# Optimization experiments

Hardware: AMD Instinct MI355X
Metric: run time of the kernel (lower is better)

Reference implementation:

```python
import jax, jax.numpy as jnp
import numpy as np

B, S, F, D, H, DFF, C = 64, 1024, 136, 64, 2, 256, 2
DH = D // H


def sinusoidal_pe(seq_len, d_model):
    position = jnp.arange(seq_len, dtype=jnp.float32)[:, None]
    div_term = jnp.exp(jnp.arange(0, d_model, 2, dtype=jnp.float32) * (-np.log(10000.0) / d_model))
    ang = position * div_term  # [S, D/2]
    pe = jnp.zeros((seq_len, d_model), dtype=jnp.float32)
    pe = pe.at[:, 0::2].set(jnp.sin(ang))
    pe = pe.at[:, 1::2].set(jnp.cos(ang))
    return pe


def layer_norm(x, g, b, eps=1e-5):
    mu = jnp.mean(x, axis=-1, keepdims=True)
    var = jnp.mean(jnp.square(x - mu), axis=-1, keepdims=True)
    return (x - mu) * jax.lax.rsqrt(var + eps) * g + b


def setup_inputs() -> dict:
    key = jax.random.key(0)
    ks = jax.random.split(key, 16)
    r = lambda k, shape, scale: jax.random.normal(k, shape, dtype=jnp.float32) * scale
    return {
        'x': r(ks[0], (B, S, F), 1.0),
        'W_in': r(ks[1], (F, D), F ** -0.5), 'b_in': jnp.zeros((D,), jnp.float32),
        'W_qkv': r(ks[2], (D, 3 * D), D ** -0.5), 'b_qkv': jnp.zeros((3 * D,), jnp.float32),
        'W_o': r(ks[3], (D, D), D ** -0.5), 'b_o': jnp.zeros((D,), jnp.float32),
        'g1': jnp.ones((D,), jnp.float32), 'beta1': jnp.zeros((D,), jnp.float32),
        'W1': r(ks[4], (D, DFF), D ** -0.5), 'b1': jnp.zeros((DFF,), jnp.float32),
        'W2': r(ks[5], (DFF, D), DFF ** -0.5), 'b2': jnp.zeros((D,), jnp.float32),
        'g2': jnp.ones((D,), jnp.float32), 'beta2': jnp.zeros((D,), jnp.float32),
        'W_c1': r(ks[6], (D, D), D ** -0.5), 'b_c1': jnp.zeros((D,), jnp.float32),
        'W_c2': r(ks[7], (D, C), D ** -0.5), 'b_c2': jnp.zeros((C,), jnp.float32),
    }


def reference(x, W_in, b_in, W_qkv, b_qkv, W_o, b_o, g1, beta1, W1, b1, W2, b2, g2, beta2, W_c1, b_c1, W_c2, b_c2):
    # input projection + positional encoding
    h = x @ W_in + b_in                      # [B,S,D]
    h = h + sinusoidal_pe(h.shape[1], D)
    # multi-head self-attention with explicit weights (need_weights=True path)
    qkv = h @ W_qkv + b_qkv                  # [B,S,3D]
    q, k, v = jnp.split(qkv, 3, axis=-1)
    q = q.reshape(B, S, H, DH)
    k = k.reshape(B, S, H, DH)
    v = v.reshape(B, S, H, DH)
    scores = jnp.einsum('bihd,bjhd->bhij', q, k) / np.sqrt(DH)
    attn = jax.nn.softmax(scores, axis=-1)   # [B,H,S,S] per-head attention weights
    ctx = jnp.einsum('bhij,bjhd->bihd', attn, v).reshape(B, S, D)
    attn_out = ctx @ W_o + b_o
    # post-norm encoder layer (dropout inactive in eval)
    h = layer_norm(h + attn_out, g1, beta1)
    ff = jax.nn.relu(h @ W1 + b1) @ W2 + b2
    h = layer_norm(h + ff, g2, beta2)
    # mean pool + classifier
    pooled = jnp.mean(h, axis=1)             # [B,D]
    logits = jax.nn.relu(pooled @ W_c1 + b_c1) @ W_c2 + b_c2
    return logits, attn
```

## Files before the change

### kernel.cpp

```cpp
#include <hip/hip_runtime.h>


typedef unsigned short u16;
typedef short bf16x8 __attribute__((ext_vector_type(8)));
typedef short bf16x4 __attribute__((ext_vector_type(4)));
typedef float f32x4 __attribute__((ext_vector_type(4)));

#define DEVI __device__ __forceinline__
#define MFMA __builtin_amdgcn_mfma_f32_16x16x32_bf16

DEVI u16 f2bf(float f) {
  union { float f; unsigned u; } v; v.f = f;
  unsigned r = v.u + 0x7FFFu + ((v.u >> 16) & 1u);
  return (u16)(r >> 16);
}
DEVI float bf2f(u16 h) {
  union { unsigned u; float f; } v; v.u = ((unsigned)h) << 16;
  return v.f;
}
DEVI float wred_sum(float v) {
#pragma unroll
  for (int off = 32; off; off >>= 1) v += __shfl_xor(v, off);
  return v;
}

__global__ __launch_bounds__(256) void r1_inproj(const float* __restrict__ x,
                                                 const float* __restrict__ Win,
                                                 const float* __restrict__ bin,
                                                 float* __restrict__ hf) {
  __shared__ float xs[32][140];
  const int r0 = blockIdx.x * 32, t = threadIdx.x;
  const int lane = t & 63, wv = t >> 6;
  for (int e = t; e < 32 * 136; e += 256) {
    int r = e / 136, k = e - r * 136;
    xs[r][k] = x[(size_t)(r0 + r) * 136 + k];
  }
  __syncthreads();
  float acc[8];
#pragma unroll
  for (int r = 0; r < 8; ++r) acc[r] = 0.f;
  for (int k = 0; k < 136; k += 4) {
    float w0 = Win[(size_t)k * 64 + lane];
    float w1 = Win[(size_t)(k + 1) * 64 + lane];
    float w2 = Win[(size_t)(k + 2) * 64 + lane];
    float w3 = Win[(size_t)(k + 3) * 64 + lane];
#pragma unroll
    for (int r = 0; r < 8; ++r) {
      f32x4 xv = *(const f32x4*)&xs[wv * 8 + r][k];
      acc[r] = fmaf(xv[0], w0, fmaf(xv[1], w1, fmaf(xv[2], w2, fmaf(xv[3], w3, acc[r]))));
    }
  }
  const float bcol = bin[lane];
  const int m = lane >> 1;
  const float freq = __expf((float)(2 * m) * -0.14391156831212787f);
  const int s0 = r0 & 1023;
#pragma unroll
  for (int r = 0; r < 8; ++r) {
    const int row = wv * 8 + r;
    const float ang = (float)(s0 + row) * freq;
    const float pe = (lane & 1) ? cosf(ang) : sinf(ang);
    hf[(size_t)(r0 + row) * 64 + lane] = acc[r] + bcol + pe;
  }
}

__global__ __launch_bounds__(384) void r2_qkv(const float* __restrict__ hf,
                                              const float* __restrict__ Wq,
                                              const float* __restrict__ bq,
                                              u16* __restrict__ qH, u16* __restrict__ qL,
                                              u16* __restrict__ kH, u16* __restrict__ kL,
                                              u16* __restrict__ vtH, u16* __restrict__ vtL) {
  __shared__ float hr[32][68];
  __shared__ u16 vbH[64][40];
  __shared__ u16 vbL[64][40];
  const int r0 = blockIdx.x * 32, t = threadIdx.x;
  const int g = t / 192, u = t - g * 192;
  for (int e = t; e < 2048; e += 384) {
    int r = e >> 6, k = e & 63;
    hr[r][k] = hf[(size_t)(r0 + r) * 64 + k];
  }
  __syncthreads();
  float acc[16];
  const float bias = bq[u];
#pragma unroll
  for (int r = 0; r < 16; ++r) acc[r] = bias;
  for (int k = 0; k < 64; k += 4) {
    float w0 = Wq[(size_t)k * 192 + u];
    float w1 = Wq[(size_t)(k + 1) * 192 + u];
    float w2 = Wq[(size_t)(k + 2) * 192 + u];
    float w3 = Wq[(size_t)(k + 3) * 192 + u];
#pragma unroll
    for (int r = 0; r < 16; ++r) {
      f32x4 hv = *(const f32x4*)&hr[g * 16 + r][k];
      acc[r] = fmaf(hv[0], w0, fmaf(hv[1], w1, fmaf(hv[2], w2, fmaf(hv[3], w3, acc[r]))));
    }
  }
  const int which = u >> 6, c = u & 63, h = c >> 5, dh = c & 31;
  const int b = r0 >> 10, s0 = r0 & 1023;
  const size_t bh = (size_t)(b * 2 + h);
#pragma unroll
  for (int r = 0; r < 16; ++r) {
    const int row = g * 16 + r;
    const int s = s0 + row;
    u16 hi = f2bf(acc[r]);
    u16 lo = f2bf(acc[r] - bf2f(hi));
    if (which == 0)      { qH[(bh * 1024 + s) * 32 + dh] = hi; qL[(bh * 1024 + s) * 32 + dh] = lo; }
    else if (which == 1) { kH[(bh * 1024 + s) * 32 + dh] = hi; kL[(bh * 1024 + s) * 32 + dh] = lo; }
    else                 { vbH[c][row] = hi; vbL[c][row] = lo; }
  }
  __syncthreads();
  if (t < 128) {
    const int hh = (t & 63) >> 5, dh2 = t & 31;
    const size_t vb = ((size_t)(b * 2 + hh) * 32 + dh2) * 1024 + s0;
    const u16* src = (t < 64) ? &vbH[(t & 63)][0] : &vbL[(t & 63)][0];
    u16* dst = (t < 64) ? vtH : vtL;
#pragma unroll
    for (int i = 0; i < 2; ++i) {
      bf16x8 v = *(const bf16x8*)&src[i * 16];
      bf16x8 w = *(const bf16x8*)&src[i * 16 + 8];
      *(bf16x8*)&dst[vb + i * 16] = v;
      *(bf16x8*)&dst[vb + i * 16 + 8] = w;
    }
  }
}

__global__ __launch_bounds__(512, 4) void r3_fa(const u16* __restrict__ qH, const u16* __restrict__ qL,
                                                const u16* __restrict__ kH, const u16* __restrict__ kL,
                                                const u16* __restrict__ vtH, const u16* __restrict__ vtL,
                                                float* __restrict__ attn, float* __restrict__ ctx) {
  __shared__ __align__(16) char smem[33280];
  u16* pb = (u16*)smem;
  float* reds = (float*)(smem + 32768);
  float* part = (float*)smem;

  const int bid = blockIdx.x;
  const int wid = (bid & 7) * 1024 + (bid >> 3);
  const int bh = wid >> 6, qt = wid & 63;
  const int t = threadIdx.x, lane = t & 63, wv = t >> 6;
  const int fr = lane & 15, rg = lane >> 4, koff = rg * 8;
  const int i0 = qt * 16;
  const float scale = 0.17677669529663687f;

  const size_t qoff = ((size_t)bh * 1024 + i0 + fr) * 32 + koff;
  bf16x8 aqh = *(const bf16x8*)&qH[qoff];
  bf16x8 aql = *(const bf16x8*)&qL[qoff];

  f32x4 s[8];
#pragma unroll
  for (int jl = 0; jl < 8; ++jl) {
    const int jt = wv * 8 + jl;
    const size_t kof = ((size_t)bh * 1024 + jt * 16 + fr) * 32 + koff;
    bf16x8 bkh = *(const bf16x8*)&kH[kof];
    bf16x8 bkl = *(const bf16x8*)&kL[kof];
    f32x4 a = {};
    a = MFMA(aqh, bkh, a, 0, 0, 0);
    a = MFMA(aqh, bkl, a, 0, 0, 0);
    a = MFMA(aql, bkh, a, 0, 0, 0);
#pragma unroll
    for (int r = 0; r < 4; ++r) s[jl][r] = a[r] * scale;
  }

  float s4[4] = {0.f, 0.f, 0.f, 0.f};
#pragma unroll
  for (int jl = 0; jl < 8; ++jl)
#pragma unroll
    for (int r = 0; r < 4; ++r) { s[jl][r] = __expf(s[jl][r]); s4[r] += s[jl][r]; }
#pragma unroll
  for (int off = 1; off < 16; off <<= 1)
#pragma unroll
    for (int r = 0; r < 4; ++r) s4[r] += __shfl_xor(s4[r], off);
  if (fr == 0) {
#pragma unroll
    for (int r = 0; r < 4; ++r) reds[wv * 16 + rg * 4 + r] = s4[r];
  }
  __syncthreads();
  float inv[4];
#pragma unroll
  for (int r = 0; r < 4; ++r) {
    const int row = rg * 4 + r;
    float ssum = reds[row];
#pragma unroll
    for (int w = 1; w < 8; ++w) ssum += reds[w * 16 + row];
    inv[r] = 1.f / ssum;
  }

#pragma unroll
  for (int r = 0; r < 4; ++r) {
    const int row = rg * 4 + r;
    const int sw = rg << 4;
    const int rb = row * 1024;
#pragma unroll
    for (int jl = 0; jl < 8; jl += 2) {
      const float f0 = s[jl][r] * inv[r];
      const float f1 = s[jl + 1][r] * inv[r];
      unsigned pk;
      asm("v_cvt_pk_bf16_f32 %0, %1, %2" : "=v"(pk) : "v"(f0), "v"(f1));
      const int c0 = (wv * 8 + jl) * 16 + fr;
      pb[rb + (c0 ^ sw)] = (u16)pk;
      pb[rb + ((c0 + 16) ^ sw)] = (u16)(pk >> 16);
    }
  }
  __syncthreads();

  {
    const int row = t >> 5, x32 = t & 31;
    const int sw = (row >> 2) << 4;
    const size_t gb = ((size_t)bh * 1024 + i0 + row) * 1024;
#pragma unroll
    for (int c = 0; c < 8; ++c) {
      const int col = x32 * 4 + 128 * c;
      bf16x4 v = *(const bf16x4*)&pb[row * 1024 + (col ^ sw)];
      f32x4 o;
#pragma unroll
      for (int i = 0; i < 4; ++i) o[i] = bf2f((u16)v[i]);
      __builtin_nontemporal_store(o, (f32x4*)&attn[gb + col]);
    }
  }

  const int sw2 = (fr >> 2) << 4;
  f32x4 acc2[2] = {};
#pragma unroll
  for (int i = 0; i < 4; ++i) {
    const int kt = wv * 4 + i;
    const int cb = kt * 32 + rg * 8;
    bf16x8 ph = *(const bf16x8*)&pb[fr * 1024 + (cb ^ sw2)];
#pragma unroll
    for (int nb = 0; nb < 2; ++nb) {
      const size_t vo = ((size_t)bh * 32 + nb * 16 + fr) * 1024 + cb;
      bf16x8 vh = *(const bf16x8*)&vtH[vo];
      bf16x8 vl = *(const bf16x8*)&vtL[vo];
      acc2[nb] = MFMA(ph, vh, acc2[nb], 0, 0, 0);
      acc2[nb] = MFMA(ph, vl, acc2[nb], 0, 0, 0);
    }
  }
  __syncthreads();
#pragma unroll
  for (int nb = 0; nb < 2; ++nb)
#pragma unroll
    for (int r = 0; r < 4; ++r)
      part[(wv * 16 + rg * 4 + r) * 32 + nb * 16 + fr] = acc2[nb][r];
  __syncthreads();
  const int b = bh >> 1, h = bh & 1;
  {
    const int row = t >> 5, dh = t & 31;
    float v = part[(row) * 32 + dh];
#pragma unroll
    for (int w = 1; w < 8; ++w) v += part[(w * 16 + row) * 32 + dh];
    ctx[((size_t)b * 1024 + i0 + row) * 64 + h * 32 + dh] = v;
  }
}

__global__ __launch_bounds__(256) void r56_ln_ff(const float* __restrict__ ctx,
                                                 const float* __restrict__ Wo,
                                                 const float* __restrict__ bo,
                                                 const float* __restrict__ hf,
                                                 const float* __restrict__ g1,
                                                 const float* __restrict__ be1,
                                                 const float* __restrict__ W1,
                                                 const float* __restrict__ b1,
                                                 const float* __restrict__ W2,
                                                 const float* __restrict__ b2,
                                                 const float* __restrict__ g2,
                                                 const float* __restrict__ be2,
                                                 float* __restrict__ pp) {
  __shared__ __align__(16) char smem[38656];
  float* yr   = (float*)smem;
  float* fr   = (float*)(smem + 4352);
  float* part = (float*)(smem + 21248);
  float* cr   = (float*)(smem + 4352);
  float* wo   = (float*)(smem + 8704);
  float* pw   = (float*)(smem + 37632);
  const int r0 = blockIdx.x * 16;
  const int t = threadIdx.x, d = t & 63, wv = t >> 6;

  for (int e = t; e < 1024; e += 256) cr[(e >> 6) * 68 + (e & 63)] = ctx[(size_t)(r0 + (e >> 6)) * 64 + (e & 63)];
  for (int e = t; e < 4096; e += 256) wo[e] = Wo[e];
  __syncthreads();

  {
    float acc[4];
    const float bias = bo[d];
#pragma unroll
    for (int r = 0; r < 4; ++r) acc[r] = bias;
    for (int k = 0; k < 64; ++k) {
      const float w = wo[k * 64 + d];
#pragma unroll
      for (int r = 0; r < 4; ++r) acc[r] = fmaf(cr[(wv * 4 + r) * 68 + k], w, acc[r]);
    }
    const float gd = g1[d], bd = be1[d];
#pragma unroll
    for (int r = 0; r < 4; ++r) {
      const int row = wv * 4 + r;
      const float rv = hf[(size_t)(r0 + row) * 64 + d] + acc[r];
      const float mu = wred_sum(rv) * (1.f / 64.f);
      const float dd = rv - mu;
      const float var = wred_sum(dd * dd) * (1.f / 64.f);
      yr[row * 68 + d] = dd * rsqrtf(var + 1e-5f) * gd + bd;
    }
  }
  __syncthreads();

  {
    float acc[16];
    const float bias = b1[t];
#pragma unroll
    for (int r = 0; r < 16; ++r) acc[r] = bias;
    for (int k = 0; k < 64; k += 4) {
      float w0 = W1[(size_t)k * 256 + t];
      float w1 = W1[(size_t)(k + 1) * 256 + t];
      float w2 = W1[(size_t)(k + 2) * 256 + t];
      float w3 = W1[(size_t)(k + 3) * 256 + t];
#pragma unroll
      for (int r = 0; r < 16; ++r) {
        f32x4 yv = *(const f32x4*)&yr[r * 68 + k];
        acc[r] = fmaf(yv[0], w0, fmaf(yv[1], w1, fmaf(yv[2], w2, fmaf(yv[3], w3, acc[r]))));
      }
    }
#pragma unroll
    for (int r = 0; r < 16; ++r) fr[r * 264 + t] = fmaxf(acc[r], 0.f);
  }
  __syncthreads();

  {
    float acc[16];
#pragma unroll
    for (int r = 0; r < 16; ++r) acc[r] = 0.f;
    for (int kk = 0; kk < 64; kk += 4) {
      const int k = wv * 64 + kk;
      float w0 = W2[(size_t)k * 64 + d];
      float w1 = W2[(size_t)(k + 1) * 64 + d];
      float w2 = W2[(size_t)(k + 2) * 64 + d];
      float w3 = W2[(size_t)(k + 3) * 64 + d];
#pragma unroll
      for (int r = 0; r < 16; ++r) {
        f32x4 fv = *(const f32x4*)&fr[r * 264 + k];
        acc[r] = fmaf(fv[0], w0, fmaf(fv[1], w1, fmaf(fv[2], w2, fmaf(fv[3], w3, acc[r]))));
      }
    }
#pragma unroll
    for (int r = 0; r < 16; ++r) part[(wv * 16 + r) * 64 + d] = acc[r];
  }
  __syncthreads();

  {
    float pool = 0.f;
    const float bd2 = b2[d], gd = g2[d], bd = be2[d];
#pragma unroll
    for (int rr = 0; rr < 4; ++rr) {
      const int row = wv * 4 + rr;
      const float o2 = part[row * 64 + d] + part[(16 + row) * 64 + d] +
                       part[(32 + row) * 64 + d] + part[(48 + row) * 64 + d] + bd2;
      const float rv = yr[row * 68 + d] + o2;
      const float mu = wred_sum(rv) * (1.f / 64.f);
      const float dd = rv - mu;
      const float var = wred_sum(dd * dd) * (1.f / 64.f);
      pool += dd * rsqrtf(var + 1e-5f) * gd + bd;
    }
    pw[wv * 64 + d] = pool;
  }
  __syncthreads();
  if (t < 64) pp[(size_t)blockIdx.x * 64 + t] = pw[t] + pw[64 + t] + pw[128 + t] + pw[192 + t];
}

__global__ __launch_bounds__(256) void r7_cls(const float* __restrict__ pp,
                                              const float* __restrict__ Wc1,
                                              const float* __restrict__ bc1,
                                              const float* __restrict__ Wc2,
                                              const float* __restrict__ bc2,
                                              float* __restrict__ outp) {
  __shared__ float red[4][64];
  const int b = blockIdx.x, t = threadIdx.x;
  const int lane = t & 63, wv = t >> 6;
  float po = 0.f;
  for (int i = wv; i < 64; i += 4) po += pp[(size_t)(b * 64 + i) * 64 + lane];
  red[wv][lane] = po;
  __syncthreads();
  if (wv == 0) {
    po = (red[0][lane] + red[1][lane] + red[2][lane] + red[3][lane]) * (1.f / 1024.f);
    float acc = bc1[lane];
    for (int k = 0; k < 64; ++k) acc = fmaf(__shfl(po, k), Wc1[(size_t)k * 64 + lane], acc);
    const float t1 = fmaxf(acc, 0.f);
    const float l0 = wred_sum(t1 * Wc2[(size_t)lane * 2 + 0]);
    const float l1 = wred_sum(t1 * Wc2[(size_t)lane * 2 + 1]);
    if (lane == 0) {
      outp[b * 2 + 0] = l0 + bc2[0];
      outp[b * 2 + 1] = l1 + bc2[1];
    }
  }
}

extern "C" void kernel_launch(void* const* d_in, const int* in_sizes, int n_in,
                              void* d_out, int out_size, void* d_ws, size_t ws_size,
                              hipStream_t stream) {
  (void)in_sizes; (void)n_in; (void)out_size; (void)ws_size;
  const float* x     = (const float*)d_in[0];
  const float* W_in  = (const float*)d_in[1];
  const float* b_in  = (const float*)d_in[2];
  const float* W_qkv = (const float*)d_in[3];
  const float* b_qkv = (const float*)d_in[4];
  const float* W_o   = (const float*)d_in[5];
  const float* b_o   = (const float*)d_in[6];
  const float* g1    = (const float*)d_in[7];
  const float* be1   = (const float*)d_in[8];
  const float* W1    = (const float*)d_in[9];
  const float* b1    = (const float*)d_in[10];
  const float* W2    = (const float*)d_in[11];
  const float* b2    = (const float*)d_in[12];
  const float* g2    = (const float*)d_in[13];
  const float* be2   = (const float*)d_in[14];
  const float* Wc1   = (const float*)d_in[15];
  const float* bc1   = (const float*)d_in[16];
  const float* Wc2   = (const float*)d_in[17];
  const float* bc2   = (const float*)d_in[18];

  char* ws = (char*)d_ws;
  const size_t SZF = (size_t)65536 * 64 * 4;
  const size_t SZH = (size_t)128 * 1024 * 32 * 2;
  float* hf  = (float*)(ws + 0);
  u16* qH    = (u16*)(ws + SZF);
  u16* qL    = (u16*)(ws + SZF + 1 * SZH);
  u16* kH    = (u16*)(ws + SZF + 2 * SZH);
  u16* kL    = (u16*)(ws + SZF + 3 * SZH);
  u16* vtH   = (u16*)(ws + SZF + 4 * SZH);
  u16* vtL   = (u16*)(ws + SZF + 5 * SZH);
  float* ctx = (float*)(ws + SZF + 6 * SZH);
  float* pp  = (float*)(ws + 2 * SZF + 6 * SZH);

  float* outp = (float*)d_out;
  float* attn = outp + 128;

  r1_inproj<<<2048, 256, 0, stream>>>(x, W_in, b_in, hf);
  r2_qkv   <<<2048, 384, 0, stream>>>(hf, W_qkv, b_qkv, qH, qL, kH, kL, vtH, vtL);
  r3_fa    <<<8192, 512, 0, stream>>>(qH, qL, kH, kL, vtH, vtL, attn, ctx);
  r56_ln_ff<<<4096, 256, 0, stream>>>(ctx, W_o, b_o, hf, g1, be1, W1, b1, W2, b2, g2, be2, pp);
  r7_cls   <<<64, 256, 0, stream>>>(pp, Wc1, bc1, Wc2, bc2, outp);
}
```

Measured before the change: 415.0 us.

## Move Wo/FFN GEMMs to bf16x3 MFMA with pre-split transposed weights

Adds a prep kernel that transposes W_o, W1 and W2 and splits each into bf16 hi/lo pairs. The fused out-proj + LayerNorm + FFN kernel then runs all three GEMMs with 16x16x32 bf16 MFMA using the three-product hi/lo split, in place of scalar FP32 FMAs. This aims to cut ALU time in the FFN stage, which the attention kernel likely dominates. The cost is an extra launch, more LDS conversion work, and slightly reduced precision from dropping the lo*lo term.

New measurement: 377.8 us. 9.0% less time.

```diff
diff --git a/kernel.cpp b/kernel.cpp
--- a/kernel.cpp
+++ b/kernel.cpp
@@ -22,6 +22,33 @@
 #pragma unroll
   for (int off = 32; off; off >>= 1) v += __shfl_xor(v, off);
   return v;
+}
+
+__global__ __launch_bounds__(256) void k_prep(const float* __restrict__ Wo,
+                                              const float* __restrict__ W1,
+                                              const float* __restrict__ W2,
+                                              u16* __restrict__ WoTH, u16* __restrict__ WoTL,
+                                              u16* __restrict__ W1TH, u16* __restrict__ W1TL,
+                                              u16* __restrict__ W2TH, u16* __restrict__ W2TL) {
+  const int id = blockIdx.x * 256 + threadIdx.x;
+  if (id < 4096) {
+    const int n = id >> 6, k = id & 63;
+    const float v = Wo[(size_t)k * 64 + n];
+    const u16 hi = f2bf(v);
+    WoTH[id] = hi; WoTL[id] = f2bf(v - bf2f(hi));
+  } else if (id < 20480) {
+    const int e = id - 4096;
+    const int n = e >> 6, k = e & 63;
+    const float v = W1[(size_t)k * 256 + n];
+    const u16 hi = f2bf(v);
+    W1TH[e] = hi; W1TL[e] = f2bf(v - bf2f(hi));
+  } else if (id < 36864) {
+    const int e = id - 20480;
+    const int n = e >> 8, k = e & 255;
+    const float v = W2[(size_t)k * 64 + n];
+    const u16 hi = f2bf(v);
+    W2TH[e] = hi; W2TL[e] = f2bf(v - bf2f(hi));
+  }
 }
 
 __global__ __launch_bounds__(256) void r1_inproj(const float* __restrict__ x,
@@ -250,112 +277,153 @@
 }
 
 __global__ __launch_bounds__(256) void r56_ln_ff(const float* __restrict__ ctx,
-                                                 const float* __restrict__ Wo,
+                                                 const u16* __restrict__ WoTH, const u16* __restrict__ WoTL,
                                                  const float* __restrict__ bo,
                                                  const float* __restrict__ hf,
                                                  const float* __restrict__ g1,
                                                  const float* __restrict__ be1,
-                                                 const float* __restrict__ W1,
+                                                 const u16* __restrict__ W1TH, const u16* __restrict__ W1TL,
                                                  const float* __restrict__ b1,
-                                                 const float* __restrict__ W2,
+                                                 const u16* __restrict__ W2TH, const u16* __restrict__ W2TL,
                                                  const float* __restrict__ b2,
                                                  const float* __restrict__ g2,
                                                  const float* __restrict__ be2,
                                                  float* __restrict__ pp) {
-  __shared__ __align__(16) char smem[38656];
-  float* yr   = (float*)smem;
-  float* fr   = (float*)(smem + 4352);
-  float* part = (float*)(smem + 21248);
-  float* cr   = (float*)(smem + 4352);
-  float* wo   = (float*)(smem + 8704);
-  float* pw   = (float*)(smem + 37632);
-  const int r0 = blockIdx.x * 16;
-  const int t = threadIdx.x, d = t & 63, wv = t >> 6;
-
-  for (int e = t; e < 1024; e += 256) cr[(e >> 6) * 68 + (e & 63)] = ctx[(size_t)(r0 + (e >> 6)) * 64 + (e & 63)];
-  for (int e = t; e < 4096; e += 256) wo[e] = Wo[e];
-  __syncthreads();
-
-  {
-    float acc[4];
-    const float bias = bo[d];
-#pragma unroll
-    for (int r = 0; r < 4; ++r) acc[r] = bias;
-    for (int k = 0; k < 64; ++k) {
-      const float w = wo[k * 64 + d];
-#pragma unroll
-      for (int r = 0; r < 4; ++r) acc[r] = fmaf(cr[(wv * 4 + r) * 68 + k], w, acc[r]);
-    }
-    const float gd = g1[d], bd = be1[d];
+  __shared__ __align__(16) char smem[31232];
+  u16* crH = (u16*)smem;
+  u16* crL = (u16*)(smem + 2304);
+  u16* fH  = (u16*)smem;
+  u16* fL  = (u16*)(smem + 8448);
+  float* rr = (float*)(smem + 16896);
+  float* yr = (float*)(smem + 21248);
+  u16* yH  = (u16*)(smem + 25600);
+  u16* yL  = (u16*)(smem + 27904);
+  float* pw = (float*)(smem + 30208);
+
+  const int r0 = blockIdx.x * 16, t = threadIdx.x;
+  const int lane = t & 63, wv = t >> 6;
+  const int fr = lane & 15, rg = lane >> 4, koff = rg * 8;
+
+  for (int e = t; e < 1024; e += 256) {
+    const int r = e >> 6, c = e & 63;
+    const float v = ctx[(size_t)(r0 + r) * 64 + c];
+    const u16 hi = f2bf(v);
+    crH[r * 72 + c] = hi;
+    crL[r * 72 + c] = f2bf(v - bf2f(hi));
+  }
+  __syncthreads();
+
+  {
+    f32x4 acc = {};
+#pragma unroll
+    for (int kt = 0; kt < 2; ++kt) {
+      bf16x8 aH = *(const bf16x8*)&crH[fr * 72 + kt * 32 + koff];
+      bf16x8 aL = *(const bf16x8*)&crL[fr * 72 + kt * 32 + koff];
+      const size_t wb = (size_t)(wv * 16 + fr) * 64 + kt * 32 + koff;
+      bf16x8 bH = *(const bf16x8*)&WoTH[wb];
+      bf16x8 bL = *(const bf16x8*)&WoTL[wb];
+      acc = MFMA(aH, bH, acc, 0, 0, 0);
+      acc = MFMA(aH, bL, acc, 0, 0, 0);
+      acc = MFMA(aL, bH, acc, 0, 0, 0);
+    }
+    const int col = wv * 16 + fr;
+    const float bias = bo[col];
+#pragma unroll
+    for (int r = 0; r < 4; ++r) {
+      const int row = rg * 4 + r;
+      rr[row * 68 + col] = acc[r] + bias + hf[(size_t)(r0 + row) * 64 + col];
+    }
+  }
+  __syncthreads();
+
+  {
+    const float gd = g1[lane], bd = be1[lane];
 #pragma unroll
     for (int r = 0; r < 4; ++r) {
       const int row = wv * 4 + r;
-      const float rv = hf[(size_t)(r0 + row) * 64 + d] + acc[r];
+      const float rv = rr[row * 68 + lane];
       const float mu = wred_sum(rv) * (1.f / 64.f);
       const float dd = rv - mu;
       const float var = wred_sum(dd * dd) * (1.f / 64.f);
-      yr[row * 68 + d] = dd * rsqrtf(var + 1e-5f) * gd + bd;
-    }
-  }
-  __syncthreads();
-
-  {
-    float acc[16];
-    const float bias = b1[t];
-#pragma unroll
-    for (int r = 0; r < 16; ++r) acc[r] = bias;
-    for (int k = 0; k < 64; k += 4) {
-      float w0 = W1[(size_t)k * 256 + t];
-      float w1 = W1[(size_t)(k + 1) * 256 + t];
-      float w2 = W1[(size_t)(k + 2) * 256 + t];
-      float w3 = W1[(size_t)(k + 3) * 256 + t];
-#pragma unroll
-      for (int r = 0; r < 16; ++r) {
-        f32x4 yv = *(const f32x4*)&yr[r * 68 + k];
-        acc[r] = fmaf(yv[0], w0, fmaf(yv[1], w1, fmaf(yv[2], w2, fmaf(yv[3], w3, acc[r]))));
+      const float y = dd * rsqrtf(var + 1e-5f) * gd + bd;
+      yr[row * 68 + lane] = y;
+      const u16 hi = f2bf(y);
+      yH[row * 72 + lane] = hi;
+      yL[row * 72 + lane] = f2bf(y - bf2f(hi));
+    }
+  }
+  __syncthreads();
+
+  {
+    bf16x8 aH0 = *(const bf16x8*)&yH[fr * 72 + koff];
+    bf16x8 aL0 = *(const bf16x8*)&yL[fr * 72 + koff];
+    bf16x8 aH1 = *(const bf16x8*)&yH[fr * 72 + 32 + koff];
+    bf16x8 aL1 = *(const bf16x8*)&yL[fr * 72 + 32 + koff];
+#pragma unroll
+    for (int c = 0; c < 4; ++c) {
+      const int ct = wv * 4 + c;
+      const size_t wb = (size_t)(ct * 16 + fr) * 64;
+      bf16x8 bH0 = *(const bf16x8*)&W1TH[wb + koff];
+      bf16x8 bL0 = *(const bf16x8*)&W1TL[wb + koff];
+      bf16x8 bH1 = *(const bf16x8*)&W1TH[wb + 32 + koff];
+      bf16x8 bL1 = *(const bf16x8*)&W1TL[wb + 32 + koff];
+      f32x4 acc = {};
+      acc = MFMA(aH0, bH0, acc, 0, 0, 0);
+      acc = MFMA(aH0, bL0, acc, 0, 0, 0);
+      acc = MFMA(aL0, bH0, acc, 0, 0, 0);
+      acc = MFMA(aH1, bH1, acc, 0, 0, 0);
+      acc = MFMA(aH1, bL1, acc, 0, 0, 0);
+      acc = MFMA(aL1, bH1, acc, 0, 0, 0);
+      const int col = ct * 16 + fr;
+      const float bias = b1[col];
+#pragma unroll
+      for (int r = 0; r < 4; ++r) {
+        const int row = rg * 4 + r;
+        const float v = fmaxf(acc[r] + bias, 0.f);
+        const u16 hi = f2bf(v);
+        fH[row * 264 + col] = hi;
+        fL[row * 264 + col] = f2bf(v - bf2f(hi));
       }
     }
-#pragma unroll
-    for (int r = 0; r < 16; ++r) fr[r * 264 + t] = fmaxf(acc[r], 0.f);
-  }
-  __syncthreads();
-
-  {
-    float acc[16];
-#pragma unroll
-    for (int r = 0; r < 16; ++r) acc[r] = 0.f;
-    for (int kk = 0; kk < 64; kk += 4) {
-      const int k = wv * 64 + kk;
-      float w0 = W2[(size_t)k * 64 + d];
-      float w1 = W2[(size_t)(k + 1) * 64 + d];
-      float w2 = W2[(size_t)(k + 2) * 64 + d];
-      float w3 = W2[(size_t)(k + 3) * 64 + d];
-#pragma unroll
-      for (int r = 0; r < 16; ++r) {
-        f32x4 fv = *(const f32x4*)&fr[r * 264 + k];
-        acc[r] = fmaf(fv[0], w0, fmaf(fv[1], w1, fmaf(fv[2], w2, fmaf(fv[3], w3, acc[r]))));
-      }
-    }
-#pragma unroll
-    for (int r = 0; r < 16; ++r) part[(wv * 16 + r) * 64 + d] = acc[r];
+  }
+  __syncthreads();
+
+  {
+    f32x4 acc = {};
+#pragma unroll
+    for (int kt = 0; kt < 8; ++kt) {
+      bf16x8 aH = *(const bf16x8*)&fH[fr * 264 + kt * 32 + koff];
+      bf16x8 aL = *(const bf16x8*)&fL[fr * 264 + kt * 32 + koff];
+      const size_t wb = (size_t)(wv * 16 + fr) * 256 + kt * 32 + koff;
+      bf16x8 bH = *(const bf16x8*)&W2TH[wb];
+      bf16x8 bL = *(const bf16x8*)&W2TL[wb];
+      acc = MFMA(aH, bH, acc, 0, 0, 0);
+      acc = MFMA(aH, bL, acc, 0, 0, 0);
+      acc = MFMA(aL, bH, acc, 0, 0, 0);
+    }
+    const int col = wv * 16 + fr;
+    const float bias = b2[col];
+#pragma unroll
+    for (int r = 0; r < 4; ++r) {
+      const int row = rg * 4 + r;
+      rr[row * 68 + col] = acc[r] + bias + yr[row * 68 + col];
+    }
   }
   __syncthreads();
 
   {
     float pool = 0.f;
-    const float bd2 = b2[d], gd = g2[d], bd = be2[d];
-#pragma unroll
-    for (int rr = 0; rr < 4; ++rr) {
-      const int row = wv * 4 + rr;
-      const float o2 = part[row * 64 + d] + part[(16 + row) * 64 + d] +
-                       part[(32 + row) * 64 + d] + part[(48 + row) * 64 + d] + bd2;
-      const float rv = yr[row * 68 + d] + o2;
+    const float gd = g2[lane], bd = be2[lane];
+#pragma unroll
+    for (int r = 0; r < 4; ++r) {
+      const int row = wv * 4 + r;
+      const float rv = rr[row * 68 + lane];
       const float mu = wred_sum(rv) * (1.f / 64.f);
       const float dd = rv - mu;
       const float var = wred_sum(dd * dd) * (1.f / 64.f);
       pool += dd * rsqrtf(var + 1e-5f) * gd + bd;
     }
-    pw[wv * 64 + d] = pool;
+    pw[wv * 64 + lane] = pool;
   }
   __syncthreads();
   if (t < 64) pp[(size_t)blockIdx.x * 64 + t] = pw[t] + pw[64 + t] + pw[128 + t] + pw[192 + t];
@@ -424,13 +492,22 @@
   u16* vtL   = (u16*)(ws + SZF + 5 * SZH);
   float* ctx = (float*)(ws + SZF + 6 * SZH);
   float* pp  = (float*)(ws + 2 * SZF + 6 * SZH);
+  char*  wsp = ws + 2 * SZF + 6 * SZH + (size_t)1048576;
+  u16* WoTH  = (u16*)(wsp);
+  u16* WoTL  = (u16*)(wsp + 8192);
+  u16* W1TH  = (u16*)(wsp + 16384);
+  u16* W1TL  = (u16*)(wsp + 49152);
+  u16* W2TH  = (u16*)(wsp + 81920);
+  u16* W2TL  = (u16*)(wsp + 114688);
 
   float* outp = (float*)d_out;
   float* attn = outp + 128;
 
+  k_prep   <<<144, 256, 0, stream>>>(W_o, W1, W2, WoTH, WoTL, W1TH, W1TL, W2TH, W2TL);
   r1_inproj<<<2048, 256, 0, stream>>>(x, W_in, b_in, hf);
   r2_qkv   <<<2048, 384, 0, stream>>>(hf, W_qkv, b_qkv, qH, qL, kH, kL, vtH, vtL);
   r3_fa    <<<8192, 512, 0, stream>>>(qH, qL, kH, kL, vtH, vtL, attn, ctx);
-  r56_ln_ff<<<4096, 256, 0, stream>>>(ctx, W_o, b_o, hf, g1, be1, W1, b1, W2, b2, g2, be2, pp);
+  r56_ln_ff<<<4096, 256, 0, stream>>>(ctx, WoTH, WoTL, b_o, hf, g1, be1,
+                                      W1TH, W1TL, b1, W2TH, W2TL, b2, g2, be2, pp);
   r7_cls   <<<64, 256, 0, stream>>>(pp, Wc1, bc1, Wc2, bc2, outp);
 }
```
